# Kernel tuning notes

Hardware: AMD Instinct MI355X
Metric: run time of the kernel (lower is better)

Reference implementation:

```python
import jax, jax.numpy as jnp
import numpy as np

DECAY = 0.99
EPS_VQ = 1e-5
EPS_LN = 1e-5


def setup_inputs() -> dict:
    key = jax.random.key(0)
    ks = jax.random.split(key, 6)
    N, DIN, D, K = 32768, 1024, 512, 1024
    return {
        "x": jax.random.normal(ks[0], (N, DIN), dtype=jnp.float32),
        "enc_w": jax.random.normal(ks[1], (DIN, D), dtype=jnp.float32) * (1.0 / np.sqrt(DIN)),
        "enc_b": jnp.zeros((D,), jnp.float32),
        "ln_g": jnp.ones((D,), jnp.float32),
        "ln_b": jnp.zeros((D,), jnp.float32),
        "dec_w": jax.random.normal(ks[2], (D, DIN), dtype=jnp.float32) * (1.0 / np.sqrt(D)),
        "dec_b": jnp.zeros((DIN,), jnp.float32),
        "embeddings": jax.random.normal(ks[3], (K, D), dtype=jnp.float32),
        "cluster_size": jnp.ones((K,), jnp.float32),
        "ema_embed_sum": jax.random.normal(ks[4], (K, D), dtype=jnp.float32),
    }


def _layernorm(h, g, b):
    mu = jnp.mean(h, axis=-1, keepdims=True)
    var = jnp.var(h, axis=-1, keepdims=True)
    return (h - mu) * jax.lax.rsqrt(var + EPS_LN) * g + b


def reference(x, enc_w, enc_b, ln_g, ln_b, dec_w, dec_b, embeddings, cluster_size, ema_embed_sum):
    K = embeddings.shape[0]
    # encoder: Linear + LayerNorm
    z_e = _layernorm(x @ enc_w + enc_b, ln_g, ln_b)  # [N, D]
    # pairwise squared L2 distances, expanded GEMM form (same argmin as (z-e)^2.sum)
    d = (jnp.sum(z_e * z_e, axis=1, keepdims=True)
         - 2.0 * (z_e @ embeddings.T)
         + jnp.sum(embeddings * embeddings, axis=1)[None, :])  # [N, K]
    indices = jnp.argmin(d, axis=1)  # [N]
    z_q = embeddings[indices]  # gather [N, D]
    # EMA codebook update (training path; buffers, no grad)
    zd = jax.lax.stop_gradient(z_e)
    counts = jax.ops.segment_sum(jnp.ones_like(indices, jnp.float32), indices, num_segments=K)
    embed_sum = jax.ops.segment_sum(zd, indices, num_segments=K)  # one_hot.T @ z
    new_cluster_size = DECAY * cluster_size + (1.0 - DECAY) * counts
    new_ema_embed_sum = DECAY * ema_embed_sum + (1.0 - DECAY) * embed_sum
    n = jnp.sum(new_cluster_size)
    cs = (new_cluster_size + EPS_VQ) / (n + K * EPS_VQ) * n
    new_embeddings = new_ema_embed_sum / cs[:, None]
    # commitment loss + straight-through estimator
    commit_loss = jnp.mean((z_e - jax.lax.stop_gradient(z_q)) ** 2)
    z_q_st = z_e + jax.lax.stop_gradient(z_q - z_e)
    x_recon = z_q_st @ dec_w + dec_b
    return (x_recon, commit_loss, indices, z_e, z_q_st,
            new_embeddings, new_cluster_size, new_ema_embed_sum)
```

## Files before the change

### kernel.cpp

```cpp
#include <hip/hip_runtime.h>

typedef unsigned long long u64;
typedef unsigned int u32;
typedef _Float16 f16;
typedef _Float16 f16x8 __attribute__((ext_vector_type(8)));
typedef float f32x4 __attribute__((ext_vector_type(4)));

#define MFMA16(a, b, c) __builtin_amdgcn_mfma_f32_16x16x32_f16(a, b, c, 0, 0, 0)

#define NROWS 32768
#define DIN   1024
#define DM    512
#define KC    1024
#define SPLIT_SC  1024.0f
#define SPLIT_INV 0.0009765625f
#define CHSZ  32
#define MAXCH 2048
#define MARGIN 0.5f

#define OFF_XR   0ull
#define OFF_CL   33554432ull
#define OFF_IDX  33554433ull
#define OFF_ZE   33587201ull
#define OFF_ZQ   50364417ull
#define OFF_NE   67141633ull
#define OFF_NCS  67665921ull
#define OFF_NEMA 67666945ull

#define WS_ZNORM   2359296ull
#define WS_IDX     2490368ull
#define WS_COUNTS  2621440ull
#define WS_STARTS  2625536ull
#define WS_OFFW    2629632ull
#define WS_ROWLIST 2633728ull
#define WS_CSD     2764800ull
#define WS_ENORM   2769920ull
#define WS2_CAND   (4ull<<20)
#define WS2_WT1    (36ull<<20)
#define WS2_WT2    (37ull<<20)
#define WS2_DT     (38ull<<20)
#define WS2_E1     (39ull<<20)
#define WS3_CHPFX  (41ull<<20)
#define WS3_CHCODE ((41ull<<20) + 8192)
#define WS3_CPART  ((41ull<<20) + 16384)
#define WS3_PART   ((41ull<<20) + 65536)

__device__ inline void gload16(const f16* g, f16* l) {
  __builtin_amdgcn_global_load_lds((const __attribute__((address_space(1))) void*)g,
                                   (__attribute__((address_space(3))) void*)l, 16, 0, 0);
}

__device__ inline f16x8 ldfrag32(const f16* p, int row, int kc) {
  return *(const f16x8*)(p + row * 32 + ((kc ^ ((row >> 1) & 3)) << 3));
}

__device__ inline void stage32(const f16* gbase, int ld, int row0, int k0,
                               f16* lds, int t) {
  int r = t >> 2, c = t & 3;
  int cs = c ^ ((r >> 1) & 3);
  gload16(gbase + (size_t)(row0 + r) * ld + k0 + cs * 8, lds + t * 8);
}

__device__ inline void stageA256(const f16* gbase, int ld, int row0, int k0,
                                 f16* lds, int t) {
#pragma unroll
  for (int h = 0; h < 2; h++) {
    int e = t + h * 512;
    int r = e >> 2, c = e & 3;
    int cs = c ^ ((r >> 1) & 3);
    gload16(gbase + (size_t)(row0 + r) * ld + k0 + cs * 8, lds + e * 8);
  }
}

#define BAR2      { asm volatile("s_waitcnt lgkmcnt(0)" ::: "memory"); \
                    __builtin_amdgcn_s_barrier(); \
                    asm volatile("" ::: "memory"); }

__device__ inline u32 enc_score(float s) {
  u32 kb = __float_as_uint(s);
  return (kb & 0x80000000u) ? ~kb : (kb | 0x80000000u);
}
__device__ inline float dec_score(u32 u) {
  u32 b = (u & 0x80000000u) ? (u & 0x7fffffffu) : ~u;
  return __uint_as_float(b);
}

__global__ __launch_bounds__(256) void k_prep(const float* __restrict__ enc_w,
                                              const float* __restrict__ dec_w,
                                              const float* __restrict__ emb,
                                              f16* __restrict__ wt1,
                                              f16* __restrict__ wt2,
                                              f16* __restrict__ dT,
                                              f16* __restrict__ e1,
                                              float* __restrict__ enorm,
                                              int* __restrict__ counts) {
  __shared__ float tile[32][33];
  int bid = blockIdx.x, t = threadIdx.x;
  if (bid < 1024) {
    const float* W;
    f16 *o1, *o2;
    int K, N, bx, by;
    if (bid < 512) {
      W = enc_w; o1 = wt1; o2 = wt2; K = DIN; N = DM;
      bx = bid & 15; by = bid >> 4;
    } else {
      int b2 = bid - 512;
      W = dec_w; o1 = dT; o2 = nullptr; K = DM; N = DIN;
      bx = b2 & 31; by = b2 >> 5;
    }
    int tx = t & 31, ty = t >> 5;
    int nb = bx * 32, kb = by * 32;
#pragma unroll
    for (int i = 0; i < 32; i += 8)
      tile[ty + i][tx] = W[(size_t)(kb + ty + i) * N + nb + tx];
    __syncthreads();
#pragma unroll
    for (int i = 0; i < 32; i += 8) {
      float v = tile[tx][ty + i];
      f16 h = (f16)v;
      size_t o = (size_t)(nb + ty + i) * K + kb + tx;
      o1[o] = h;
      if (o2) o2[o] = (f16)((v - (float)h) * SPLIT_SC);
    }
  } else if (bid < 1536) {
    int tid = (bid - 1024) * 256 + t;
    for (int i = tid; i < KC * DM; i += 131072) e1[i] = (f16)emb[i];
  } else if (bid < 1792) {
    int k = (bid - 1536) * 4 + (t >> 6), lane = t & 63;
    float s = 0.f;
#pragma unroll
    for (int j = 0; j < 8; j++) {
      float v = emb[(size_t)k * DM + lane + j * 64];
      s = fmaf(v, v, s);
    }
#pragma unroll
    for (int m = 1; m < 64; m <<= 1) s += __shfl_xor(s, m, 64);
    if (lane == 0) enorm[k] = s;
  } else {
    int i = (bid - 1792) * 256 + t;
    if (i < KC) counts[i] = 0;
  }
}

__global__ __launch_bounds__(512) void k_genc4(const float* __restrict__ x,
                                               const f16* __restrict__ wt1,
                                               const f16* __restrict__ wt2,
                                               const float* __restrict__ bias,
                                               float* __restrict__ dst) {
  __shared__ __align__(16) f16 A1[128 * 32], A2[128 * 32];
  __shared__ __align__(16) f16 B1[2][128 * 32], B2[2][128 * 32];
  int t = threadIdx.x, lane = t & 63, wid = t >> 6;
  int wm = wid >> 2, wn = wid & 3;
  int l = blockIdx.x;
  int xcd = l & 7, s = l >> 3, ct = s & 3;
  int p = ((s >> 2) << 3) | xcd;
  int m0 = p * 128, n0 = ct * 128;
  int r = t >> 2, cg = t & 3;
  int cslot = cg ^ ((r >> 1) & 3);
  const float* ax = x + (size_t)(m0 + r) * DIN + cg * 8;
  f32x4 accA[4][2] = {}, accB[4][2] = {};

#define GCONV(v0, v1)                                                       \
  {                                                                         \
    float a_[8] = {v0.x, v0.y, v0.z, v0.w, v1.x, v1.y, v1.z, v1.w};         \
    f16 h1_[8], h2_[8];                                                     \
    _Pragma("unroll") for (int j_ = 0; j_ < 8; j_++) {                      \
      f16 h_ = (f16)a_[j_];                                                 \
      h1_[j_] = h_;                                                         \
      h2_[j_] = (f16)((a_[j_] - (float)h_) * SPLIT_SC);                     \
    }                                                                       \
    *(f16x8*)(A1 + r * 32 + cslot * 8) = *(f16x8*)h1_;                      \
    *(f16x8*)(A2 + r * 32 + cslot * 8) = *(f16x8*)h2_;                      \
  }

#define GCOMP(buf)                                                          \
  {                                                                         \
    int kc_ = lane >> 4;                                                    \
    f16x8 a1f[4], a2f[4], b1f[2], b2f[2];                                   \
    _Pragma("unroll") for (int m_ = 0; m_ < 4; m_++) {                      \
      int row_ = wm * 64 + m_ * 16 + (lane & 15);                           \
      a1f[m_] = ldfrag32(A1, row_, kc_);                                    \
      a2f[m_] = ldfrag32(A2, row_, kc_);                                    \
    }                                                                       \
    _Pragma("unroll") for (int n_ = 0; n_ < 2; n_++) {                      \
      int row_ = wn * 32 + n_ * 16 + (lane & 15);                           \
      b1f[n_] = ldfrag32(B1[buf], row_, kc_);                               \
      b2f[n_] = ldfrag32(B2[buf], row_, kc_);                               \
    }                                                                       \
    _Pragma("unroll") for (int m_ = 0; m_ < 4; m_++)                        \
      _Pragma("unroll") for (int n_ = 0; n_ < 2; n_++) {                    \
        accA[m_][n_] = MFMA16(a1f[m_], b1f[n_], accA[m_][n_]);              \
        accB[m_][n_] = MFMA16(a1f[m_], b2f[n_], accB[m_][n_]);              \
        accB[m_][n_] = MFMA16(a2f[m_], b1f[n_], accB[m_][n_]);              \
      }                                                                     \
  }

  float4 c0 = *(const float4*)(ax);
  float4 c1 = *(const float4*)(ax + 4);
  float4 n0v = *(const float4*)(ax + 32);
  float4 n1v = *(const float4*)(ax + 36);
  stage32(wt1, DIN, n0, 0, B1[0], t);
  stage32(wt2, DIN, n0, 0, B2[0], t);
  asm volatile("s_waitcnt vmcnt(4)" ::: "memory");

  for (int it = 0; it < 32; ++it) {
    GCONV(c0, c1);
    if (it + 1 < 32) {
      stage32(wt1, DIN, n0, (it + 1) * 32, B1[(it + 1) & 1], t);
      stage32(wt2, DIN, n0, (it + 1) * 32, B2[(it + 1) & 1], t);
    }
    float4 f0, f1;
    if (it + 2 < 32) {
      f0 = *(const float4*)(ax + (it + 2) * 32);
      f1 = *(const float4*)(ax + (it + 2) * 32 + 4);
    }
    if (it <= 29) {
      asm volatile("s_waitcnt vmcnt(4) lgkmcnt(0)" ::: "memory");
    } else if (it == 30) {
      asm volatile("s_waitcnt vmcnt(2) lgkmcnt(0)" ::: "memory");
    } else {
      asm volatile("s_waitcnt vmcnt(0) lgkmcnt(0)" ::: "memory");
    }
    __builtin_amdgcn_sched_barrier(0);
    __builtin_amdgcn_s_barrier();
    asm volatile("" ::: "memory");
    GCOMP(it & 1);
    BAR2;
    c0 = n0v; c1 = n1v; n0v = f0; n1v = f1;
  }
#undef GCONV
#undef GCOMP

#pragma unroll
  for (int m = 0; m < 4; m++)
#pragma unroll
    for (int n = 0; n < 2; n++)
#pragma unroll
      for (int j = 0; j < 4; j++) {
        int row = m0 + wm * 64 + m * 16 + (lane >> 4) * 4 + j;
        int col = n0 + wn * 32 + n * 16 + (lane & 15);
        dst[(size_t)row * DM + col] = accA[m][n][j] + SPLIT_INV * accB[m][n][j] + bias[col];
      }
}

__global__ __launch_bounds__(512, 4) void k_dist4(const f16* __restrict__ z1,
                                                  const f16* __restrict__ e1,
                                                  const float* __restrict__ enorm,
                                                  u64* __restrict__ cand) {
  __shared__ __align__(16) f16 A[3][256 * 32];
  __shared__ __align__(16) f16 B[3][128 * 32];
  int t = threadIdx.x, lane = t & 63, wid = t >> 6;
  int wr = wid >> 1, wc = wid & 1;
  int l = blockIdx.x;
  int xcd = l & 7, s = l >> 3, ct = s & 7;
  int p = ((s >> 3) << 3) | xcd;
  int r0 = p * 256, c0 = ct * 128;
  f32x4 acc[4][4] = {};
  int kc = lane >> 4;

  stageA256(z1, DM, r0, 0, A[0], t);
  stage32(e1, DM, c0, 0, B[0], t);

  for (int it = 0; it < 16; ++it) {
    int buf = it % 3;
    if (it < 15) {
      int nb = (it + 1) % 3;
      int k0n = (it + 1) * 32;
      stageA256(z1, DM, r0, k0n, A[nb], t);
      stage32(e1, DM, c0, k0n, B[nb], t);
      asm volatile("s_waitcnt vmcnt(3)" ::: "memory");
    } else {
      asm volatile("s_waitcnt vmcnt(0)" ::: "memory");
    }
    __builtin_amdgcn_sched_barrier(0);
    __builtin_amdgcn_s_barrier();
    asm volatile("" ::: "memory");
    f16x8 af[4], bf[4];
#pragma unroll
    for (int m = 0; m < 4; m++)
      af[m] = ldfrag32(A[buf], wr * 64 + m * 16 + (lane & 15), kc);
#pragma unroll
    for (int n = 0; n < 4; n++)
      bf[n] = ldfrag32(B[buf], wc * 64 + n * 16 + (lane & 15), kc);
#pragma unroll
    for (int m = 0; m < 4; m++)
#pragma unroll
      for (int n = 0; n < 4; n++) acc[m][n] = MFMA16(af[m], bf[n], acc[m][n]);
  }

  __syncthreads();
  u64 (*cand_s)[4] = (u64 (*)[4])(&A[0][0]);
  float en[4];
#pragma unroll
  for (int n = 0; n < 4; n++)
    en[n] = enorm[c0 + wc * 64 + n * 16 + (lane & 15)];
#pragma unroll
  for (int m = 0; m < 4; m++)
#pragma unroll
    for (int j = 0; j < 4; j++) {
      int r_l = wr * 64 + m * 16 + (lane >> 4) * 4 + j;
      u64 lo = ~0ull, hi = ~0ull;
#pragma unroll
      for (int n = 0; n < 4; n++) {
        int col = c0 + wc * 64 + n * 16 + (lane & 15);
        float sc = fmaf(-2.0f, acc[m][n][j], en[n]);
        u64 k = ((u64)enc_score(sc) << 32) | (u32)col;
        if (k < lo) { hi = lo; lo = k; }
        else if (k < hi) { hi = k; }
      }
#pragma unroll
      for (int msk = 1; msk < 16; msk <<= 1) {
        u64 lo2 = __shfl_xor(lo, msk, 64);
        u64 hi2 = __shfl_xor(hi, msk, 64);
        u64 nlo = lo < lo2 ? lo : lo2;
        u64 losr = lo < lo2 ? lo2 : lo;
        u64 nh = hi < hi2 ? hi : hi2;
        hi = losr < nh ? losr : nh;
        lo = nlo;
      }
      if ((lane & 15) == 0) {
        cand_s[r_l][wc * 2] = lo;
        cand_s[r_l][wc * 2 + 1] = hi;
      }
    }
  __syncthreads();
  if (t < 256) {
    u64 b0 = ~0ull, b1 = ~0ull;
#pragma unroll
    for (int i = 0; i < 4; i++) {
      u64 k = cand_s[t][i];
      if (k < b0) { b1 = b0; b0 = k; }
      else if (k < b1) { b1 = k; }
    }
    u64* dst = cand + ((size_t)(r0 + t) * 16 + ct * 2);
    dst[0] = b0;
    dst[1] = b1;
  }
}

__global__ __launch_bounds__(512, 4) void k_gdec4(const f16* __restrict__ e1,
                                                  const int* __restrict__ idxws,
                                                  const f16* __restrict__ dT,
                                                  const float* __restrict__ bias,
                                                  float* __restrict__ dst) {
  __shared__ __align__(16) f16 A[3][256 * 32];
  __shared__ __align__(16) f16 B[3][128 * 32];
  int t = threadIdx.x, lane = t & 63, wid = t >> 6;
  int wr = wid >> 1, wc = wid & 1;
  int l = blockIdx.x;
  int xcd = l & 7, s = l >> 3, ct = s & 7;
  int p = ((s >> 3) << 3) | xcd;
  int r0 = p * 256, c0 = ct * 128;
  f32x4 acc[4][4] = {};
  int kc = lane >> 4;

  int rlo = t >> 2, clo = t & 3;
  int cs0 = clo ^ ((rlo >> 1) & 3);
  int i0 = idxws[r0 + rlo];
  int i1 = idxws[r0 + 128 + rlo];
  const f16* ga0 = e1 + (size_t)i0 * DM + cs0 * 8;
  const f16* ga1 = e1 + (size_t)i1 * DM + cs0 * 8;

  gload16(ga0, A[0] + t * 8);
  gload16(ga1, A[0] + (t + 512) * 8);
  stage32(dT, DM, c0, 0, B[0], t);

  for (int it = 0; it < 16; ++it) {
    int buf = it % 3;
    if (it < 15) {
      int nb = (it + 1) % 3;
      int k0n = (it + 1) * 32;
      gload16(ga0 + k0n, A[nb] + t * 8);
      gload16(ga1 + k0n, A[nb] + (t + 512) * 8);
      stage32(dT, DM, c0, k0n, B[nb], t);
      asm volatile("s_waitcnt vmcnt(3)" ::: "memory");
    } else {
      asm volatile("s_waitcnt vmcnt(0)" ::: "memory");
    }
    __builtin_amdgcn_sched_barrier(0);
    __builtin_amdgcn_s_barrier();
    asm volatile("" ::: "memory");
    f16x8 af[4], bf[4];
#pragma unroll
    for (int m = 0; m < 4; m++)
      af[m] = ldfrag32(A[buf], wr * 64 + m * 16 + (lane & 15), kc);
#pragma unroll
    for (int n = 0; n < 4; n++)
      bf[n] = ldfrag32(B[buf], wc * 64 + n * 16 + (lane & 15), kc);
#pragma unroll
    for (int m = 0; m < 4; m++)
#pragma unroll
      for (int n = 0; n < 4; n++) acc[m][n] = MFMA16(af[m], bf[n], acc[m][n]);
  }

#pragma unroll
  for (int m = 0; m < 4; m++)
#pragma unroll
    for (int n = 0; n < 4; n++)
#pragma unroll
      for (int j = 0; j < 4; j++) {
        int row = r0 + wr * 64 + m * 16 + (lane >> 4) * 4 + j;
        int col = c0 + wc * 64 + n * 16 + (lane & 15);
        dst[(size_t)row * DIN + col] = acc[m][n][j] + bias[col];
      }
}

__global__ __launch_bounds__(256) void k_resolve(const u64* __restrict__ cand,
                                                 const float* __restrict__ znorm,
                                                 const float* __restrict__ enorm,
                                                 const float* __restrict__ emb,
                                                 float* __restrict__ out,
                                                 int* __restrict__ idxws,
                                                 int* __restrict__ counts,
                                                 float* __restrict__ cpart) {
  int t = threadIdx.x, bid = blockIdx.x;
  int r0 = bid * 16;
  __shared__ u64 key_s[256];
  __shared__ int idx_s[16];
  __shared__ float commit_s[16];
  __shared__ int flagcnt_s;
  __shared__ int flagrow_s[16];
  key_s[t] = cand[(size_t)r0 * 16 + t];
  if (t == 0) flagcnt_s = 0;
  __syncthreads();

  if (t < 16) {
    u64 best = ~0ull;
#pragma unroll
    for (int i = 0; i < 16; i++) {
      u64 k = key_s[t * 16 + i];
      best = k < best ? k : best;
    }
    float smin = dec_score((u32)(best >> 32));
    float thr = smin + MARGIN;
    int nc = 0;
#pragma unroll
    for (int i = 0; i < 16; i++)
      if (dec_score((u32)(key_s[t * 16 + i] >> 32)) <= thr) nc++;
    idx_s[t] = (int)(u32)(best & 0xffffffffull);
    commit_s[t] = znorm[r0 + t] + smin;
    if (nc > 1) {
      int pz = atomicAdd(&flagcnt_s, 1);
      flagrow_s[pz] = t;
    }
  }
  __syncthreads();

  if (t < 64) {
    int nf = flagcnt_s;
    for (int fi = 0; fi < nf; fi++) {
      int lr = flagrow_s[fi];
      int R = r0 + lr;
      u64 amin = ~0ull;
      for (int i = 0; i < 16; i++) {
        u64 k = key_s[lr * 16 + i];
        amin = k < amin ? k : amin;
      }
      float thr = dec_score((u32)(amin >> 32)) + MARGIN;
      float zn = znorm[R];
      const float* z = out + OFF_ZE + (size_t)R * DM;
      u64 bestk = ~0ull;
      for (int i = 0; i < 16; i++) {
        u64 k = key_s[lr * 16 + i];
        if (dec_score((u32)(k >> 32)) > thr) continue;
        int c = (int)(u32)(k & 0xffffffffull);
        const float* e = emb + (size_t)c * DM;
        float pdot = 0.f;
#pragma unroll
        for (int j = 0; j < 8; j++) pdot = fmaf(z[t + j * 64], e[t + j * 64], pdot);
#pragma unroll
        for (int m = 1; m < 64; m <<= 1) pdot += __shfl_xor(pdot, m, 64);
        float d = fmaf(-2.0f, pdot, zn) + enorm[c];
        u64 pk = ((u64)enc_score(d) << 32) | (u32)c;
        bestk = pk < bestk ? pk : bestk;
      }
      if (t == 0) {
        idx_s[lr] = (int)(u32)(bestk & 0xffffffffull);
        commit_s[lr] = dec_score((u32)(bestk >> 32));
      }
    }
  }
  __syncthreads();

  if (t < 16) {
    int R = r0 + t;
    int idx = idx_s[t];
    out[OFF_IDX + R] = (float)idx;
    idxws[R] = idx;
    atomicAdd(counts + idx, 1);
  }
  __syncthreads();
  for (int rr = 0; rr < 16; rr++) {
    int R = r0 + rr;
    const float* e = emb + (size_t)idx_s[rr] * DM;
    float* zq = out + OFF_ZQ + (size_t)R * DM;
#pragma unroll
    for (int j = 0; j < 2; j++) {
      int c = t + j * 256;
      zq[c] = e[c];
    }
  }
  if (t == 0) {
    float s = 0.f;
#pragma unroll
    for (int i = 0; i < 16; i++) s += commit_s[i];
    cpart[bid] = s;
  }
}

__global__ __launch_bounds__(256) void k_ln3(float* __restrict__ ze,
                                             const float* __restrict__ g,
                                             const float* __restrict__ b,
                                             f16* __restrict__ z1,
                                             float* __restrict__ znorm) {
  int t = threadIdx.x, lane = t & 63, wid = t >> 6;
  int R = blockIdx.x * 4 + wid;
  float* row = ze + (size_t)R * DM;
  float v[8];
  float s = 0.f, sq = 0.f;
#pragma unroll
  for (int j = 0; j < 8; j++) {
    v[j] = row[lane + j * 64];
    s += v[j];
    sq = fmaf(v[j], v[j], sq);
  }
#pragma unroll
  for (int m = 1; m < 64; m <<= 1) {
    s += __shfl_xor(s, m, 64);
    sq += __shfl_xor(sq, m, 64);
  }
  float mu = s * (1.f / DM);
  float var = sq * (1.f / DM) - mu * mu;
  float rs = rsqrtf(var + 1e-5f);
  float zn = 0.f;
#pragma unroll
  for (int j = 0; j < 8; j++) {
    int c = lane + j * 64;
    float o = (v[j] - mu) * rs * g[c] + b[c];
    row[c] = o;
    z1[(size_t)R * DM + c] = (f16)o;
    zn = fmaf(o, o, zn);
  }
#pragma unroll
  for (int m = 1; m < 64; m <<= 1) zn += __shfl_xor(zn, m, 64);
  if (lane == 0) znorm[R] = zn;
}

__global__ __launch_bounds__(1024) void k_scan(const int* __restrict__ counts,
                                               const float* __restrict__ cs_in,
                                               float* __restrict__ out,
                                               int* __restrict__ starts,
                                               int* __restrict__ offw,
                                               float* __restrict__ csd,
                                               const float* __restrict__ cpart,
                                               int* __restrict__ chpfx,
                                               int* __restrict__ chcode) {
  __shared__ float f[1024];
  __shared__ int ib[1024];
  int t = threadIdx.x;
  f[t] = cpart[t] + cpart[t + 1024];
  __syncthreads();
  for (int s = 512; s > 0; s >>= 1) {
    if (t < s) f[t] += f[t + s];
    __syncthreads();
  }
  if (t == 0) out[OFF_CL] = f[0] * (1.f / ((float)NROWS * (float)DM));
  __syncthreads();

  int cnt = counts[t];
  float ncs = 0.99f * cs_in[t] + 0.01f * (float)cnt;
  out[OFF_NCS + t] = ncs;
  f[t] = ncs;
  __syncthreads();
  for (int s = 512; s > 0; s >>= 1) {
    if (t < s) f[t] += f[t + s];
    __syncthreads();
  }
  float n = f[0];
  csd[t] = (ncs + 1e-5f) / (n + (float)KC * 1e-5f) * n;
  ib[t] = cnt;
  __syncthreads();
  for (int s = 1; s < 1024; s <<= 1) {
    int y = (t >= s) ? ib[t - s] : 0;
    __syncthreads();
    ib[t] += y;
    __syncthreads();
  }
  int excl = ib[t] - cnt;
  starts[t] = excl;
  offw[t] = excl;
  int nch = (cnt + CHSZ - 1) / CHSZ;
  __syncthreads();
  ib[t] = nch;
  __syncthreads();
  for (int s = 1; s < 1024; s <<= 1) {
    int y = (t >= s) ? ib[t - s] : 0;
    __syncthreads();
    ib[t] += y;
    __syncthreads();
  }
  int chx = ib[t] - nch;
  chpfx[t] = chx;
  if (t == KC - 1) chpfx[KC] = ib[t];
  for (int j = 0; j < nch; j++) chcode[chx + j] = t;
}

__global__ __launch_bounds__(256) void k_scatter(const int* __restrict__ idxws,
                                                 int* __restrict__ offw,
                                                 int* __restrict__ rowlist) {
  int r = blockIdx.x * 256 + threadIdx.x;
  int idx = idxws[r];
  int pos = atomicAdd(offw + idx, 1);
  rowlist[pos] = r;
}

__global__ __launch_bounds__(128) void k_partsum(const int* __restrict__ chpfx,
                                                 const int* __restrict__ chcode,
                                                 const int* __restrict__ starts,
                                                 const int* __restrict__ counts,
                                                 const int* __restrict__ rowlist,
                                                 const float* __restrict__ out,
                                                 float* __restrict__ part) {
  int c = blockIdx.x, t = threadIdx.x;
  if (c >= chpfx[KC]) return;
  int code = chcode[c];
  int j = c - chpfx[code];
  int ofs = starts[code] + j * CHSZ;
  int len = min(CHSZ, counts[code] - j * CHSZ);
  __shared__ int rl[CHSZ];
  if (t < len) rl[t] = rowlist[ofs + t];
  __syncthreads();
  const float* zeb = out + OFF_ZE;
  float a0 = 0.f, a1 = 0.f, a2 = 0.f, a3 = 0.f;
  for (int i = 0; i < len; i++) {
    const float* z = zeb + (size_t)rl[i] * DM;
    a0 += z[t];
    a1 += z[t + 128];
    a2 += z[t + 256];
    a3 += z[t + 384];
  }
  float* pp = part + (size_t)c * DM;
  pp[t] = a0;
  pp[t + 128] = a1;
  pp[t + 256] = a2;
  pp[t + 384] = a3;
}

__global__ __launch_bounds__(128) void k_codesum2(const int* __restrict__ chpfx,
                                                  const float* __restrict__ part,
                                                  const float* __restrict__ ema_in,
                                                  const float* __restrict__ csd,
                                                  float* __restrict__ out) {
  int k = blockIdx.x, t = threadIdx.x;
  int base = chpfx[k], nch = chpfx[k + 1] - base;
  float a0 = 0.f, a1 = 0.f, a2 = 0.f, a3 = 0.f;
  for (int i = 0; i < nch; i++) {
    const float* pp = part + (size_t)(base + i) * DM;
    a0 += pp[t];
    a1 += pp[t + 128];
    a2 += pp[t + 256];
    a3 += pp[t + 384];
  }
  float cs = csd[k];
  float sum[4] = {a0, a1, a2, a3};
#pragma unroll
  for (int j = 0; j < 4; j++) {
    int c = t + j * 128;
    float e = 0.99f * ema_in[(size_t)k * DM + c] + 0.01f * sum[j];
    out[OFF_NEMA + (size_t)k * DM + c] = e;
    out[OFF_NE + (size_t)k * DM + c] = e / cs;
  }
}

extern "C" void kernel_launch(void* const* d_in, const int* in_sizes, int n_in,
                              void* d_out, int out_size, void* d_ws, size_t ws_size,
                              hipStream_t stream) {
  (void)in_sizes; (void)n_in; (void)out_size; (void)ws_size;
  const float* x = (const float*)d_in[0];
  const float* enc_w = (const float*)d_in[1];
  const float* enc_b = (const float*)d_in[2];
  const float* ln_g = (const float*)d_in[3];
  const float* ln_b = (const float*)d_in[4];
  const float* dec_w = (const float*)d_in[5];
  const float* dec_b = (const float*)d_in[6];
  const float* emb = (const float*)d_in[7];
  const float* cs_in = (const float*)d_in[8];
  const float* ema_in = (const float*)d_in[9];
  float* out = (float*)d_out;
  char* ws = (char*)d_ws;
  float* znorm = (float*)(ws + WS_ZNORM);
  int* idxws = (int*)(ws + WS_IDX);
  int* counts = (int*)(ws + WS_COUNTS);
  int* starts = (int*)(ws + WS_STARTS);
  int* offw = (int*)(ws + WS_OFFW);
  int* rowlist = (int*)(ws + WS_ROWLIST);
  float* csd = (float*)(ws + WS_CSD);
  float* enorm = (float*)(ws + WS_ENORM);
  u64* cand = (u64*)(ws + WS2_CAND);
  f16* wt1 = (f16*)(ws + WS2_WT1);
  f16* wt2 = (f16*)(ws + WS2_WT2);
  f16* dT = (f16*)(ws + WS2_DT);
  f16* e1 = (f16*)(ws + WS2_E1);
  int* chpfx = (int*)(ws + WS3_CHPFX);
  int* chcode = (int*)(ws + WS3_CHCODE);
  float* cpart = (float*)(ws + WS3_CPART);
  float* part = (float*)(ws + WS3_PART);
  f16* z1 = (f16*)out;

  k_prep<<<dim3(1796), dim3(256), 0, stream>>>(enc_w, dec_w, emb, wt1, wt2, dT,
                                               e1, enorm, counts);
  k_genc4<<<dim3(1024), dim3(512), 0, stream>>>(x, wt1, wt2, enc_b, out + OFF_ZE);
  k_ln3<<<dim3(8192), dim3(256), 0, stream>>>(out + OFF_ZE, ln_g, ln_b, z1, znorm);
  k_dist4<<<dim3(1024), dim3(512), 0, stream>>>(z1, e1, enorm, cand);
  k_resolve<<<dim3(2048), dim3(256), 0, stream>>>(cand, znorm, enorm, emb, out,
                                                  idxws, counts, cpart);
  k_scan<<<dim3(1), dim3(1024), 0, stream>>>(counts, cs_in, out, starts, offw, csd,
                                             cpart, chpfx, chcode);
  k_scatter<<<dim3(NROWS / 256), dim3(256), 0, stream>>>(idxws, offw, rowlist);
  k_partsum<<<dim3(MAXCH), dim3(128), 0, stream>>>(chpfx, chcode, starts, counts,
                                                   rowlist, out, part);
  k_codesum2<<<dim3(KC), dim3(128), 0, stream>>>(chpfx, part, ema_in, csd, out);
  k_gdec4<<<dim3(1024), dim3(512), 0, stream>>>(e1, idxws, dT, dec_b, out + OFF_XR);
}
```

Measured before the change: 343.5 us.

## Precompute decoded codebook then gather rows instead of per-row decoder GEMM

Because z_q_st equals a codebook row in value, x_recon is computed as the K×DIN product of the codebook with the decoder weights plus bias, and each output row is then gathered by index. This replaces a 32768×512×1024 GEMM with a 1024×512×1024 GEMM followed by a memory-bound row copy. The decoded table reuses the candidate workspace buffer. A risk is that it differs slightly from computing z_e + (z_q - z_e) in float, and the small GEMM launches only 64 blocks.

Result: faster. 336.7 us (-2.0%).

```diff
diff --git a/kernel.cpp b/kernel.cpp
--- a/kernel.cpp
+++ b/kernel.cpp
@@ -338,31 +338,18 @@
   }
 }
 
-__global__ __launch_bounds__(512, 4) void k_gdec4(const f16* __restrict__ e1,
-                                                  const int* __restrict__ idxws,
-                                                  const f16* __restrict__ dT,
-                                                  const float* __restrict__ bias,
-                                                  float* __restrict__ dst) {
-  __shared__ __align__(16) f16 A[3][256 * 32];
-  __shared__ __align__(16) f16 B[3][128 * 32];
+__global__ __launch_bounds__(512) void k_edgemm(const f16* __restrict__ e1,
+                                                const f16* __restrict__ dT,
+                                                const float* __restrict__ bias,
+                                                float* __restrict__ ED) {
+  __shared__ __align__(16) f16 A[3][128 * 32], B[3][128 * 32];
   int t = threadIdx.x, lane = t & 63, wid = t >> 6;
-  int wr = wid >> 1, wc = wid & 1;
-  int l = blockIdx.x;
-  int xcd = l & 7, s = l >> 3, ct = s & 7;
-  int p = ((s >> 3) << 3) | xcd;
-  int r0 = p * 256, c0 = ct * 128;
-  f32x4 acc[4][4] = {};
+  int wm = wid >> 2, wn = wid & 3;
+  int r0 = (blockIdx.x >> 3) * 128, c0 = (blockIdx.x & 7) * 128;
+  f32x4 acc[4][2] = {};
   int kc = lane >> 4;
 
-  int rlo = t >> 2, clo = t & 3;
-  int cs0 = clo ^ ((rlo >> 1) & 3);
-  int i0 = idxws[r0 + rlo];
-  int i1 = idxws[r0 + 128 + rlo];
-  const f16* ga0 = e1 + (size_t)i0 * DM + cs0 * 8;
-  const f16* ga1 = e1 + (size_t)i1 * DM + cs0 * 8;
-
-  gload16(ga0, A[0] + t * 8);
-  gload16(ga1, A[0] + (t + 512) * 8);
+  stage32(e1, DM, r0, 0, A[0], t);
   stage32(dT, DM, c0, 0, B[0], t);
 
   for (int it = 0; it < 16; ++it) {
@@ -370,39 +357,53 @@
     if (it < 15) {
       int nb = (it + 1) % 3;
       int k0n = (it + 1) * 32;
-      gload16(ga0 + k0n, A[nb] + t * 8);
-      gload16(ga1 + k0n, A[nb] + (t + 512) * 8);
+      stage32(e1, DM, r0, k0n, A[nb], t);
       stage32(dT, DM, c0, k0n, B[nb], t);
-      asm volatile("s_waitcnt vmcnt(3)" ::: "memory");
+      asm volatile("s_waitcnt vmcnt(2)" ::: "memory");
     } else {
       asm volatile("s_waitcnt vmcnt(0)" ::: "memory");
     }
     __builtin_amdgcn_sched_barrier(0);
     __builtin_amdgcn_s_barrier();
     asm volatile("" ::: "memory");
-    f16x8 af[4], bf[4];
+    f16x8 af[4], bf[2];
 #pragma unroll
     for (int m = 0; m < 4; m++)
-      af[m] = ldfrag32(A[buf], wr * 64 + m * 16 + (lane & 15), kc);
-#pragma unroll
-    for (int n = 0; n < 4; n++)
-      bf[n] = ldfrag32(B[buf], wc * 64 + n * 16 + (lane & 15), kc);
+      af[m] = ldfrag32(A[buf], wm * 64 + m * 16 + (lane & 15), kc);
+#pragma unroll
+    for (int n = 0; n < 2; n++)
+      bf[n] = ldfrag32(B[buf], wn * 32 + n * 16 + (lane & 15), kc);
 #pragma unroll
     for (int m = 0; m < 4; m++)
 #pragma unroll
-      for (int n = 0; n < 4; n++) acc[m][n] = MFMA16(af[m], bf[n], acc[m][n]);
+      for (int n = 0; n < 2; n++) acc[m][n] = MFMA16(af[m], bf[n], acc[m][n]);
   }
 
 #pragma unroll
   for (int m = 0; m < 4; m++)
 #pragma unroll
-    for (int n = 0; n < 4; n++)
+    for (int n = 0; n < 2; n++)
 #pragma unroll
       for (int j = 0; j < 4; j++) {
-        int row = r0 + wr * 64 + m * 16 + (lane >> 4) * 4 + j;
-        int col = c0 + wc * 64 + n * 16 + (lane & 15);
-        dst[(size_t)row * DIN + col] = acc[m][n][j] + bias[col];
+        int row = r0 + wm * 64 + m * 16 + (lane >> 4) * 4 + j;
+        int col = c0 + wn * 32 + n * 16 + (lane & 15);
+        ED[(size_t)row * DIN + col] = acc[m][n][j] + bias[col];
       }
+}
+
+__global__ __launch_bounds__(256) void k_gatherx(const int* __restrict__ idxws,
+                                                 const float* __restrict__ ED,
+                                                 float* __restrict__ xr) {
+  int t = threadIdx.x, r0 = blockIdx.x * 16;
+  __shared__ int idx_s[16];
+  if (t < 16) idx_s[t] = idxws[r0 + t];
+  __syncthreads();
+  for (int rr = 0; rr < 16; rr++) {
+    int R = r0 + rr;
+    const float4* src = (const float4*)(ED + (size_t)idx_s[rr] * DIN);
+    float4* dst = (float4*)(xr + (size_t)R * DIN);
+    dst[t] = src[t];
+  }
 }
 
 __global__ __launch_bounds__(256) void k_resolve(const u64* __restrict__ cand,
@@ -697,6 +698,7 @@
   float* csd = (float*)(ws + WS_CSD);
   float* enorm = (float*)(ws + WS_ENORM);
   u64* cand = (u64*)(ws + WS2_CAND);
+  float* ED = (float*)(ws + WS2_CAND);
   f16* wt1 = (f16*)(ws + WS2_WT1);
   f16* wt2 = (f16*)(ws + WS2_WT2);
   f16* dT = (f16*)(ws + WS2_DT);
@@ -714,11 +716,12 @@
   k_dist4<<<dim3(1024), dim3(512), 0, stream>>>(z1, e1, enorm, cand);
   k_resolve<<<dim3(2048), dim3(256), 0, stream>>>(cand, znorm, enorm, emb, out,
                                                   idxws, counts, cpart);
+  k_edgemm<<<dim3(64), dim3(512), 0, stream>>>(e1, dT, dec_b, ED);
   k_scan<<<dim3(1), dim3(1024), 0, stream>>>(counts, cs_in, out, starts, offw, csd,
                                              cpart, chpfx, chcode);
   k_scatter<<<dim3(NROWS / 256), dim3(256), 0, stream>>>(idxws, offw, rowlist);
   k_partsum<<<dim3(MAXCH), dim3(128), 0, stream>>>(chpfx, chcode, starts, counts,
                                                    rowlist, out, part);
   k_codesum2<<<dim3(KC), dim3(128), 0, stream>>>(chpfx, part, ema_in, csd, out);
-  k_gdec4<<<dim3(1024), dim3(512), 0, stream>>>(e1, idxws, dT, dec_b, out + OFF_XR);
-}
+  k_gatherx<<<dim3(2048), dim3(256), 0, stream>>>(idxws, ED, out + OFF_XR);
+}
```
